# Performance work log

Measured on AMD Instinct MI355X. Metric: run time of the kernel, lower is better.

The kernel has to match this reference:

```python
import jax, jax.numpy as jnp
import numpy as np

B, N, KNB, F, H = 1, 50000, 16, 128, 128
BN_EPS = 1e-3  # keras BatchNormalization default epsilon
ALPHA = 0.3    # keras LeakyReLU default negative slope


def setup_inputs() -> dict:
    key = jax.random.key(0)
    ks = jax.random.split(key, 14)
    s_in = 1.0 / np.sqrt(F)
    s_cat = 1.0 / np.sqrt(F + H)
    return {
        'embeddings': jax.random.normal(ks[0], (B, N, F), jnp.float32),
        'weights': jnp.zeros((1, 1), jnp.float32),  # unused in call_att
        'neighbor_set': jax.random.randint(ks[1], (B, N, KNB), 0, N),
        'Wq': jax.random.normal(ks[2], (F, H), jnp.float32) * s_in,
        'bq': jnp.zeros((H,), jnp.float32),
        'Wk': jax.random.normal(ks[3], (F, H), jnp.float32) * s_in,
        'bk': jnp.zeros((H,), jnp.float32),
        'Wv': jax.random.normal(ks[4], (F, H), jnp.float32) * s_in,
        'bv': jnp.zeros((H,), jnp.float32),
        'W1': jax.random.normal(ks[5], (F + H, H), jnp.float32) * s_cat,
        'b1': jnp.zeros((H,), jnp.float32),
        'gamma': 1.0 + 0.1 * jax.random.normal(ks[6], (H,), jnp.float32),
        'beta': 0.1 * jax.random.normal(ks[7], (H,), jnp.float32),
        'mov_mean': 0.1 * jax.random.normal(ks[8], (H,), jnp.float32),
        'mov_var': 1.0 + 0.1 * jax.random.uniform(ks[9], (H,), jnp.float32),
    }


def reference(embeddings, weights, neighbor_set, Wq, bq, Wk, bk, Wv, bv,
              W1, b1, gamma, beta, mov_mean, mov_var):
    lrelu = lambda x: jax.nn.leaky_relu(x, ALPHA)
    # batched gather: nb[b, n, k] = embeddings[b, neighbor_set[b, n, k]]  -> [B,N,K,F]
    nb = jax.vmap(lambda e, idx: e[idx])(embeddings, neighbor_set)
    q = lrelu(embeddings @ Wq + bq)      # [B,N,H]
    k = lrelu(nb @ Wk + bk)              # [B,N,K,H]
    v = lrelu(nb @ Wv + bv)              # [B,N,K,H]
    # Q is tiled across the K neighbor rows in the original; every attention row
    # is identical, so mean-pool over rows == single-query attention. Same math.
    scores = jnp.einsum('bnh,bnkh->bnk', q, k)          # dot-product, no scale
    attn = jax.nn.softmax(scores, axis=-1)
    pooled = jnp.einsum('bnk,bnkh->bnh', attn, v)       # [B,N,H]
    h = lrelu(jnp.concatenate([embeddings, pooled], axis=-1) @ W1 + b1)
    h = h / (jnp.linalg.norm(h, axis=2, keepdims=True) + 1e-6)
    # BatchNormalization (inference form, axis=-1)
    return gamma * (h - mov_mean) * jax.lax.rsqrt(mov_var + BN_EPS) + beta
```

## Files before the change

kernel.cpp:

```cpp
#include <hip/hip_runtime.h>
#include <hip/hip_bf16.h>

#define N_NODES 50000
#define KNB 16
#define FDIM 128
#define HDIM 128
#define ALPHA 0.3f
#define BN_EPS 1e-3f

typedef __bf16 v8bf __attribute__((ext_vector_type(8)));
typedef float v4f __attribute__((ext_vector_type(4)));
typedef unsigned short ushort_t;

__device__ __forceinline__ float blo(unsigned int u) {
    union { float f; unsigned int i; } x; x.i = u << 16; return x.f;
}
__device__ __forceinline__ float bhi(unsigned int u) {
    union { float f; unsigned int i; } x; x.i = u & 0xffff0000u; return x.f;
}

__device__ __forceinline__ unsigned short f2bf(float f) {
    union { float f; unsigned int u; } x;
    x.f = f;
    unsigned int r = x.u + 0x7fffu + ((x.u >> 16) & 1u);
    return (unsigned short)(r >> 16);
}

__device__ __forceinline__ unsigned int pk2(float a, float b) {
    __hip_bfloat162 h = __float22bfloat162_rn(make_float2(a, b));
    union { __hip_bfloat162 h; unsigned int u; } r; r.h = h; return r.u;
}

__device__ __forceinline__ float lrelu(float x) { return x > 0.f ? x : ALPHA * x; }

__device__ __forceinline__ v8bf load8f(const float* p) {
    float4 A = ((const float4*)p)[0];
    float4 B = ((const float4*)p)[1];
    union { v8bf v; unsigned int u[4]; } r;
    r.u[0] = pk2(A.x, A.y); r.u[1] = pk2(A.z, A.w);
    r.u[2] = pk2(B.x, B.y); r.u[3] = pk2(B.z, B.w);
    return r.v;
}

__global__ __launch_bounds__(256) void prep_kernel(
    const float* __restrict__ Wq, const float* __restrict__ Wk,
    const float* __restrict__ Wv, const float* __restrict__ W1,
    ushort_t* __restrict__ WT)
{
    const int idx = blockIdx.x * 256 + threadIdx.x;
    if (idx < 16384) {
        int k = idx >> 7, n = idx & 127;
        WT[n * 128 + k] = f2bf(Wq[idx]);
    } else if (idx < 32768) {
        int i = idx - 16384; int k = i >> 7, n = i & 127;
        WT[16384 + n * 128 + k] = f2bf(Wk[i]);
    } else if (idx < 49152) {
        int i = idx - 32768; int k = i >> 7, n = i & 127;
        WT[32768 + n * 128 + k] = f2bf(Wv[i]);
    } else if (idx < 81920) {
        int i = idx - 49152; int k = i >> 7, n = i & 127;
        WT[49152 + n * 256 + k] = f2bf(W1[i]);
    }
}

__global__ __launch_bounds__(256) void qkv_kernel(
    const float* __restrict__ E, const ushort_t* __restrict__ WT,
    const float* __restrict__ bq, const float* __restrict__ bk,
    const float* __restrict__ bv,
    float* __restrict__ Qo, ushort_t* __restrict__ KV)
{
    __shared__ ushort_t sW[128 * 136];

    const int tid  = threadIdx.x;
    const int wave = tid >> 6;
    const int lane = tid & 63;
    const int quad = lane >> 4;
    const int j    = lane & 15;
    const int row0 = blockIdx.x * 64 + wave * 16;

    const int ar = min(row0 + j, N_NODES - 1);

    v8bf af[4];
#pragma unroll
    for (int ks = 0; ks < 4; ++ks)
        af[ks] = load8f(E + (size_t)ar * FDIM + ks * 32 + quad * 8);

    const float* biases[3] = {bq, bk, bv};

    for (int w = 0; w < 3; ++w) {
        const ushort_t* Wsrc = WT + w * 16384;
        for (int i = tid; i < 2048; i += 256) {
            int n = i >> 4, kc = i & 15;
            *(uint4*)(&sW[n * 136 + kc * 8]) = *(const uint4*)(Wsrc + n * 128 + kc * 8);
        }
        __syncthreads();

        v4f acc[8];
#pragma unroll
        for (int c = 0; c < 8; ++c) acc[c] = (v4f){0.f, 0.f, 0.f, 0.f};

#pragma unroll
        for (int ks = 0; ks < 4; ++ks) {
            const int k0 = ks * 32 + quad * 8;
            v8bf b[8];
#pragma unroll
            for (int c = 0; c < 8; ++c)
                b[c] = *(const v8bf*)(&sW[(c * 16 + j) * 136 + k0]);
#pragma unroll
            for (int c = 0; c < 8; ++c)
                acc[c] = __builtin_amdgcn_mfma_f32_16x16x32_bf16(af[ks], b[c], acc[c], 0, 0, 0);
        }

        const float* bias = biases[w];
#pragma unroll
        for (int c = 0; c < 8; ++c) {
            const int col = c * 16 + j;
            const float bv_ = bias[col];
#pragma unroll
            for (int i = 0; i < 4; ++i) {
                const int r = row0 + quad * 4 + i;
                if (r < N_NODES) {
                    const float x = lrelu(acc[c][i] + bv_);
                    if (w == 0)      Qo[(size_t)r * HDIM + col] = x;
                    else if (w == 1) KV[(size_t)r * 256 + col] = f2bf(x);
                    else             KV[(size_t)r * 256 + 128 + col] = f2bf(x);
                }
            }
        }
        __syncthreads();
    }
}

__global__ __launch_bounds__(256) void attn_kernel(
    float* __restrict__ QP, const ushort_t* __restrict__ KV,
    const int* __restrict__ nbr)
{
    const int tid  = threadIdx.x;
    const int wave = tid >> 6;
    const int lane = tid & 63;
    const int node = __builtin_amdgcn_readfirstlane(blockIdx.x * 4 + wave);

    const int t = lane >> 2;
    const int s = lane & 3;

    const int* nb = nbr + node * KNB;

    unsigned int vvals[KNB];
#pragma unroll
    for (int tt = 0; tt < KNB; ++tt) {
        int id = nb[tt];
        id = ((unsigned)id < (unsigned)N_NODES) ? id : 0;
        vvals[tt] = *(const unsigned int*)(KV + (size_t)id * 256 + 128 + 2 * lane);
    }

    int idt = nb[t];
    idt = ((unsigned)idt < (unsigned)N_NODES) ? idt : 0;
    const uint4* kbase = (const uint4*)(KV + (size_t)idt * 256 + s * 32);
    uint4 kk[4];
#pragma unroll
    for (int i = 0; i < 4; ++i) kk[i] = kbase[i];

    const float4* qbase = (const float4*)(QP + (size_t)node * HDIM + s * 32);
    float4 qv[8];
#pragma unroll
    for (int i = 0; i < 8; ++i) qv[i] = qbase[i];

    float p = 0.f;
#pragma unroll
    for (int i = 0; i < 4; ++i) {
        const float4 qa = qv[2 * i], qb = qv[2 * i + 1];
        p += qa.x * blo(kk[i].x) + qa.y * bhi(kk[i].x)
           + qa.z * blo(kk[i].y) + qa.w * bhi(kk[i].y)
           + qb.x * blo(kk[i].z) + qb.y * bhi(kk[i].z)
           + qb.z * blo(kk[i].w) + qb.w * bhi(kk[i].w);
    }
    p += __shfl_xor(p, 1, 64);
    p += __shfl_xor(p, 2, 64);

    float m = p;
    m = fmaxf(m, __shfl_xor(m, 4, 64));
    m = fmaxf(m, __shfl_xor(m, 8, 64));
    m = fmaxf(m, __shfl_xor(m, 16, 64));
    m = fmaxf(m, __shfl_xor(m, 32, 64));

    const float e = __expf(p - m);

    float sum = e;
    sum += __shfl_xor(sum, 4, 64);
    sum += __shfl_xor(sum, 8, 64);
    sum += __shfl_xor(sum, 16, 64);
    sum += __shfl_xor(sum, 32, 64);
    const float inv = 1.f / sum;

    float p0 = 0.f, p1 = 0.f;
#pragma unroll
    for (int tt = 0; tt < KNB; ++tt) {
        const float a = __shfl(e, 4 * tt, 64);
        p0 += a * blo(vvals[tt]);
        p1 += a * bhi(vvals[tt]);
    }
    ((float2*)(QP + (size_t)node * HDIM))[lane] = make_float2(p0 * inv, p1 * inv);
}

__global__ __launch_bounds__(256) void out_kernel(
    const float* __restrict__ E, const ushort_t* __restrict__ W1T,
    const float* __restrict__ b1,
    const float* __restrict__ gamma, const float* __restrict__ beta,
    const float* __restrict__ mmean, const float* __restrict__ mvar,
    float* __restrict__ OutP)
{
    __shared__ ushort_t sW[128 * 136];

    const int tid  = threadIdx.x;
    const int wave = tid >> 6;
    const int lane = tid & 63;
    const int quad = lane >> 4;
    const int j    = lane & 15;
    const int row0 = blockIdx.x * 64 + wave * 16;

    const int ar = min(row0 + j, N_NODES - 1);

    v4f acc[8];
#pragma unroll
    for (int c = 0; c < 8; ++c) acc[c] = (v4f){0.f, 0.f, 0.f, 0.f};

    for (int half = 0; half < 2; ++half) {
        for (int i = tid; i < 2048; i += 256) {
            int n = i >> 4, kc = i & 15;
            *(uint4*)(&sW[n * 136 + kc * 8]) =
                *(const uint4*)(W1T + n * 256 + half * 128 + kc * 8);
        }
        __syncthreads();

        const float* Abase = (half == 0) ? E : (const float*)OutP;
#pragma unroll
        for (int ks = 0; ks < 4; ++ks) {
            const int k0 = ks * 32 + quad * 8;
            v8bf a = load8f(Abase + (size_t)ar * 128 + k0);
            v8bf b[8];
#pragma unroll
            for (int c = 0; c < 8; ++c)
                b[c] = *(const v8bf*)(&sW[(c * 16 + j) * 136 + k0]);
#pragma unroll
            for (int c = 0; c < 8; ++c)
                acc[c] = __builtin_amdgcn_mfma_f32_16x16x32_bf16(a, b[c], acc[c], 0, 0, 0);
        }
        __syncthreads();
    }

    float scale_[8], shift_[8], bias_[8];
#pragma unroll
    for (int c = 0; c < 8; ++c) {
        const int col = c * 16 + j;
        const float sc = gamma[col] * rsqrtf(mvar[col] + BN_EPS);
        scale_[c] = sc;
        shift_[c] = beta[col] - mmean[col] * sc;
        bias_[c]  = b1[col];
    }

#pragma unroll
    for (int c = 0; c < 8; ++c)
#pragma unroll
        for (int i = 0; i < 4; ++i)
            acc[c][i] = lrelu(acc[c][i] + bias_[c]);

#pragma unroll
    for (int i = 0; i < 4; ++i) {
        float ss = 0.f;
#pragma unroll
        for (int c = 0; c < 8; ++c) ss += acc[c][i] * acc[c][i];
        ss += __shfl_xor(ss, 1, 64);
        ss += __shfl_xor(ss, 2, 64);
        ss += __shfl_xor(ss, 4, 64);
        ss += __shfl_xor(ss, 8, 64);
        const float invn = 1.f / (sqrtf(ss) + 1e-6f);
        const int r = row0 + quad * 4 + i;
        if (r < N_NODES) {
#pragma unroll
            for (int c = 0; c < 8; ++c)
                OutP[(size_t)r * HDIM + c * 16 + j] =
                    acc[c][i] * invn * scale_[c] + shift_[c];
        }
    }
}

extern "C" void kernel_launch(void* const* d_in, const int* in_sizes, int n_in,
                              void* d_out, int out_size, void* d_ws, size_t ws_size,
                              hipStream_t stream)
{
    const float* E     = (const float*)d_in[0];
    const int*   nbr   = (const int*)d_in[2];
    const float* Wq    = (const float*)d_in[3];
    const float* bq    = (const float*)d_in[4];
    const float* Wk    = (const float*)d_in[5];
    const float* bk    = (const float*)d_in[6];
    const float* Wv    = (const float*)d_in[7];
    const float* bv    = (const float*)d_in[8];
    const float* W1    = (const float*)d_in[9];
    const float* b1    = (const float*)d_in[10];
    const float* gam   = (const float*)d_in[11];
    const float* bet   = (const float*)d_in[12];
    const float* mmean = (const float*)d_in[13];
    const float* mvar  = (const float*)d_in[14];

    ushort_t* KV = (ushort_t*)d_ws;
    ushort_t* WT = KV + (size_t)N_NODES * 256;
    float* QP = (float*)d_out;

    const int gridA = (N_NODES + 63) / 64;
    prep_kernel<<<320, 256, 0, stream>>>(Wq, Wk, Wv, W1, WT);
    qkv_kernel<<<gridA, 256, 0, stream>>>(E, WT, bq, bk, bv, QP, KV);
    attn_kernel<<<N_NODES / 4, 256, 0, stream>>>(QP, KV, nbr);
    out_kernel<<<gridA, 256, 0, stream>>>(E, WT + 49152, b1, gam, bet, mmean, mvar, QP);
}
```

Before: 236.2 us.

## Fuse attention into output GEMM and read weights directly from global memory

Merges the attention kernel into the output projection kernel. Pooled vectors are computed per node into shared memory as bf16 and consumed by the MFMA GEMM, so the fp32 pooled round trip through global memory and one launch are gone. Both GEMM kernels drop the LDS weight staging and barriers, load B fragments straight from global/L2, and set launch_bounds occupancy hints. The attention step now processes one node per wave serially with per-neighbor full-wave reductions, which may cost more latency than the old four-nodes-per-block layout. Q and the output share a buffer, but each block reads only its own rows before writing them, so this is safe.

```diff
diff --git a/kernel.cpp b/kernel.cpp
--- a/kernel.cpp
+++ b/kernel.cpp
@@ -63,14 +63,12 @@
     }
 }
 
-__global__ __launch_bounds__(256) void qkv_kernel(
+__global__ __launch_bounds__(256, 4) void qkv_kernel(
     const float* __restrict__ E, const ushort_t* __restrict__ WT,
     const float* __restrict__ bq, const float* __restrict__ bk,
     const float* __restrict__ bv,
     float* __restrict__ Qo, ushort_t* __restrict__ KV)
 {
-    __shared__ ushort_t sW[128 * 136];
-
     const int tid  = threadIdx.x;
     const int wave = tid >> 6;
     const int lane = tid & 63;
@@ -89,11 +87,6 @@
 
     for (int w = 0; w < 3; ++w) {
         const ushort_t* Wsrc = WT + w * 16384;
-        for (int i = tid; i < 2048; i += 256) {
-            int n = i >> 4, kc = i & 15;
-            *(uint4*)(&sW[n * 136 + kc * 8]) = *(const uint4*)(Wsrc + n * 128 + kc * 8);
-        }
-        __syncthreads();
 
         v4f acc[8];
 #pragma unroll
@@ -105,7 +98,7 @@
             v8bf b[8];
 #pragma unroll
             for (int c = 0; c < 8; ++c)
-                b[c] = *(const v8bf*)(&sW[(c * 16 + j) * 136 + k0]);
+                b[c] = *(const v8bf*)(Wsrc + (c * 16 + j) * 128 + k0);
 #pragma unroll
             for (int c = 0; c < 8; ++c)
                 acc[c] = __builtin_amdgcn_mfma_f32_16x16x32_bf16(af[ks], b[c], acc[c], 0, 0, 0);
@@ -127,125 +120,110 @@
                 }
             }
         }
-        __syncthreads();
-    }
-}
-
-__global__ __launch_bounds__(256) void attn_kernel(
-    float* __restrict__ QP, const ushort_t* __restrict__ KV,
-    const int* __restrict__ nbr)
-{
-    const int tid  = threadIdx.x;
-    const int wave = tid >> 6;
-    const int lane = tid & 63;
-    const int node = __builtin_amdgcn_readfirstlane(blockIdx.x * 4 + wave);
-
-    const int t = lane >> 2;
-    const int s = lane & 3;
-
-    const int* nb = nbr + node * KNB;
-
-    unsigned int vvals[KNB];
-#pragma unroll
-    for (int tt = 0; tt < KNB; ++tt) {
-        int id = nb[tt];
-        id = ((unsigned)id < (unsigned)N_NODES) ? id : 0;
-        vvals[tt] = *(const unsigned int*)(KV + (size_t)id * 256 + 128 + 2 * lane);
-    }
-
-    int idt = nb[t];
-    idt = ((unsigned)idt < (unsigned)N_NODES) ? idt : 0;
-    const uint4* kbase = (const uint4*)(KV + (size_t)idt * 256 + s * 32);
-    uint4 kk[4];
-#pragma unroll
-    for (int i = 0; i < 4; ++i) kk[i] = kbase[i];
-
-    const float4* qbase = (const float4*)(QP + (size_t)node * HDIM + s * 32);
-    float4 qv[8];
-#pragma unroll
-    for (int i = 0; i < 8; ++i) qv[i] = qbase[i];
-
-    float p = 0.f;
-#pragma unroll
-    for (int i = 0; i < 4; ++i) {
-        const float4 qa = qv[2 * i], qb = qv[2 * i + 1];
-        p += qa.x * blo(kk[i].x) + qa.y * bhi(kk[i].x)
-           + qa.z * blo(kk[i].y) + qa.w * bhi(kk[i].y)
-           + qb.x * blo(kk[i].z) + qb.y * bhi(kk[i].z)
-           + qb.z * blo(kk[i].w) + qb.w * bhi(kk[i].w);
-    }
-    p += __shfl_xor(p, 1, 64);
-    p += __shfl_xor(p, 2, 64);
-
-    float m = p;
-    m = fmaxf(m, __shfl_xor(m, 4, 64));
-    m = fmaxf(m, __shfl_xor(m, 8, 64));
-    m = fmaxf(m, __shfl_xor(m, 16, 64));
-    m = fmaxf(m, __shfl_xor(m, 32, 64));
-
-    const float e = __expf(p - m);
-
-    float sum = e;
-    sum += __shfl_xor(sum, 4, 64);
-    sum += __shfl_xor(sum, 8, 64);
-    sum += __shfl_xor(sum, 16, 64);
-    sum += __shfl_xor(sum, 32, 64);
-    const float inv = 1.f / sum;
-
-    float p0 = 0.f, p1 = 0.f;
-#pragma unroll
-    for (int tt = 0; tt < KNB; ++tt) {
-        const float a = __shfl(e, 4 * tt, 64);
-        p0 += a * blo(vvals[tt]);
-        p1 += a * bhi(vvals[tt]);
-    }
-    ((float2*)(QP + (size_t)node * HDIM))[lane] = make_float2(p0 * inv, p1 * inv);
-}
-
-__global__ __launch_bounds__(256) void out_kernel(
+    }
+}
+
+__global__ __launch_bounds__(256, 4) void attn_out_kernel(
+    const float* __restrict__ Q,
+    const ushort_t* __restrict__ KV,
     const float* __restrict__ E, const ushort_t* __restrict__ W1T,
+    const int* __restrict__ nbr,
     const float* __restrict__ b1,
     const float* __restrict__ gamma, const float* __restrict__ beta,
     const float* __restrict__ mmean, const float* __restrict__ mvar,
-    float* __restrict__ OutP)
-{
-    __shared__ ushort_t sW[128 * 136];
+    float* __restrict__ Out)
+{
+    __shared__ ushort_t sPool[64 * 136];
 
     const int tid  = threadIdx.x;
     const int wave = tid >> 6;
     const int lane = tid & 63;
     const int quad = lane >> 4;
     const int j    = lane & 15;
-    const int row0 = blockIdx.x * 64 + wave * 16;
-
+    const int row0b = blockIdx.x * 64;
+
+    for (int i = 0; i < 16; ++i) {
+        const int nl = wave * 16 + i;
+        const int node = row0b + nl;
+        if (node < N_NODES) {
+            const float2 qp = ((const float2*)(Q + (size_t)node * HDIM))[lane];
+            const int* nb = nbr + node * KNB;
+
+            int ids[KNB];
+#pragma unroll
+            for (int t = 0; t < KNB; ++t) {
+                int id = nb[t];
+                ids[t] = ((unsigned)id < (unsigned)N_NODES) ? id : 0;
+            }
+
+            float sc[KNB];
+#pragma unroll
+            for (int t = 0; t < KNB; ++t) {
+                const unsigned int kp = ((const unsigned int*)(KV + (size_t)ids[t] * 256))[lane];
+                float p = qp.x * blo(kp) + qp.y * bhi(kp);
+                p += __shfl_xor(p, 32, 64);
+                p += __shfl_xor(p, 16, 64);
+                p += __shfl_xor(p, 8, 64);
+                p += __shfl_xor(p, 4, 64);
+                p += __shfl_xor(p, 2, 64);
+                p += __shfl_xor(p, 1, 64);
+                sc[t] = p;
+            }
+
+            float m = sc[0];
+#pragma unroll
+            for (int t = 1; t < KNB; ++t) m = fmaxf(m, sc[t]);
+            float sum = 0.f;
+#pragma unroll
+            for (int t = 0; t < KNB; ++t) { sc[t] = __expf(sc[t] - m); sum += sc[t]; }
+            const float inv = 1.f / sum;
+
+            float p0 = 0.f, p1 = 0.f;
+#pragma unroll
+            for (int t = 0; t < KNB; ++t) {
+                const unsigned int vp =
+                    ((const unsigned int*)(KV + (size_t)ids[t] * 256 + 128))[lane];
+                p0 += sc[t] * blo(vp);
+                p1 += sc[t] * bhi(vp);
+            }
+            *(unsigned int*)(&sPool[nl * 136 + 2 * lane]) = pk2(p0 * inv, p1 * inv);
+        } else {
+            *(unsigned int*)(&sPool[nl * 136 + 2 * lane]) = 0u;
+        }
+    }
+
+    __syncthreads();
+
+    const int row0 = row0b + wave * 16;
     const int ar = min(row0 + j, N_NODES - 1);
 
     v4f acc[8];
 #pragma unroll
     for (int c = 0; c < 8; ++c) acc[c] = (v4f){0.f, 0.f, 0.f, 0.f};
 
-    for (int half = 0; half < 2; ++half) {
-        for (int i = tid; i < 2048; i += 256) {
-            int n = i >> 4, kc = i & 15;
-            *(uint4*)(&sW[n * 136 + kc * 8]) =
-                *(const uint4*)(W1T + n * 256 + half * 128 + kc * 8);
-        }
-        __syncthreads();
-
-        const float* Abase = (half == 0) ? E : (const float*)OutP;
-#pragma unroll
-        for (int ks = 0; ks < 4; ++ks) {
-            const int k0 = ks * 32 + quad * 8;
-            v8bf a = load8f(Abase + (size_t)ar * 128 + k0);
-            v8bf b[8];
-#pragma unroll
-            for (int c = 0; c < 8; ++c)
-                b[c] = *(const v8bf*)(&sW[(c * 16 + j) * 136 + k0]);
-#pragma unroll
-            for (int c = 0; c < 8; ++c)
-                acc[c] = __builtin_amdgcn_mfma_f32_16x16x32_bf16(a, b[c], acc[c], 0, 0, 0);
-        }
-        __syncthreads();
+#pragma unroll
+    for (int ks = 0; ks < 4; ++ks) {
+        const int k0 = ks * 32 + quad * 8;
+        v8bf a = load8f(E + (size_t)ar * 128 + k0);
+        v8bf b[8];
+#pragma unroll
+        for (int c = 0; c < 8; ++c)
+            b[c] = *(const v8bf*)(W1T + (c * 16 + j) * 256 + k0);
+#pragma unroll
+        for (int c = 0; c < 8; ++c)
+            acc[c] = __builtin_amdgcn_mfma_f32_16x16x32_bf16(a, b[c], acc[c], 0, 0, 0);
+    }
+#pragma unroll
+    for (int ks = 0; ks < 4; ++ks) {
+        const int k0 = ks * 32 + quad * 8;
+        v8bf a = *(const v8bf*)(&sPool[(wave * 16 + j) * 136 + k0]);
+        v8bf b[8];
+#pragma unroll
+        for (int c = 0; c < 8; ++c)
+            b[c] = *(const v8bf*)(W1T + (c * 16 + j) * 256 + 128 + k0);
+#pragma unroll
+        for (int c = 0; c < 8; ++c)
+            acc[c] = __builtin_amdgcn_mfma_f32_16x16x32_bf16(a, b[c], acc[c], 0, 0, 0);
     }
 
     float scale_[8], shift_[8], bias_[8];
@@ -278,7 +256,7 @@
         if (r < N_NODES) {
 #pragma unroll
             for (int c = 0; c < 8; ++c)
-                OutP[(size_t)r * HDIM + c * 16 + j] =
+                Out[(size_t)r * HDIM + c * 16 + j] =
                     acc[c][i] * invn * scale_[c] + shift_[c];
         }
     }
@@ -310,6 +288,6 @@
     const int gridA = (N_NODES + 63) / 64;
     prep_kernel<<<320, 256, 0, stream>>>(Wq, Wk, Wv, W1, WT);
     qkv_kernel<<<gridA, 256, 0, stream>>>(E, WT, bq, bk, bv, QP, KV);
-    attn_kernel<<<N_NODES / 4, 256, 0, stream>>>(QP, KV, nbr);
-    out_kernel<<<gridA, 256, 0, stream>>>(E, WT + 49152, b1, gam, bet, mmean, mvar, QP);
-}
+    attn_out_kernel<<<gridA, 256, 0, stream>>>(QP, KV, E, WT + 49152, nbr,
+                                               b1, gam, bet, mmean, mvar, QP);
+}
```

After: 257.5 us. 9.1% more time.
